# Kernel tuning notes

Measured on AMD Instinct MI355X. Metric: run time of the kernel, lower is better.

Reference implementation:

```python
import jax, jax.numpy as jnp
import numpy as np

# MX microscaling spec: block_size=32 shared power-of-2 scale, int8 elements (MXINT8),
# vector (SIMD) ops rounded to bfloat16 as in microxcaling's simd_* / vec_* ops.
BLOCK = 32
BITS = 8  # int8 element format: grid step 2^(shared_exp - (BITS-2)), range [-2^(BITS-1), 2^(BITS-1)-1]


def bf16_round(x):
    # bfloat=16 rounding used by simd_split / simd_add / vec ops
    return x.astype(jnp.bfloat16).astype(jnp.float32)


def mx_quant(x):
    """MXINT8 fake-quant along last (contraction) axis with block-shared exponent.
    Straight-through estimator for gradients."""
    s = x.shape
    xb = x.reshape(s[:-1] + (s[-1] // BLOCK, BLOCK))
    amax = jnp.max(jnp.abs(xb), axis=-1, keepdims=True)
    shared_exp = jnp.floor(jnp.log2(jnp.where(amax > 0, amax, 1.0)))
    scale = jnp.exp2(shared_exp - (BITS - 2))
    q = jnp.clip(jnp.round(xb / scale), -(2.0 ** (BITS - 1)), 2.0 ** (BITS - 1) - 1) * scale
    q = jnp.where(amax > 0, q, 0.0).reshape(s)
    return x + jax.lax.stop_gradient(q - x)


def mx_linear(x, W, b):
    # quantize activations and weights to MX blocks along K, fp32 accumulate, bf16 bias-add
    y = jnp.einsum('btk,ok->bto', mx_quant(x), mx_quant(W))
    return bf16_round(y + b)


def mx_layernorm(x, w, b, eps=1e-5):
    mu = jnp.mean(x, axis=-1, keepdims=True)
    var = jnp.mean(jnp.square(x - mu), axis=-1, keepdims=True)
    return bf16_round((x - mu) * jax.lax.rsqrt(var + eps) * w + b)


def mx_gelu(x):
    # tanh-approx gelu as in microxcaling, bf16-rounded output
    c = jnp.float32(0.7978845608028654)  # sqrt(2/pi)
    return bf16_round(0.5 * x * (1.0 + jnp.tanh(c * (x + 0.044715 * x * x * x))))


def setup_inputs() -> dict:
    key = jax.random.key(0)
    ks = jax.random.split(key, 5)
    B, S, H = 2, 2048, 2048
    inputs = jax.random.normal(ks[0], (B, S, H), dtype=jnp.float32)
    ln_w = jnp.ones((H,), dtype=jnp.float32)
    ln_b = jnp.zeros((H,), dtype=jnp.float32)
    W1 = jax.random.normal(ks[1], (4 * H, H), dtype=jnp.float32) * (1.0 / np.sqrt(H))
    b1 = jnp.zeros((4 * H,), dtype=jnp.float32)
    W2 = jax.random.normal(ks[2], (H, 4 * H), dtype=jnp.float32) * (1.0 / np.sqrt(4 * H))
    b2 = jnp.zeros((H,), dtype=jnp.float32)
    return {"inputs": inputs, "ln_w": ln_w, "ln_b": ln_b, "W1": W1, "b1": b1, "W2": W2, "b2": b2}


def reference(inputs, ln_w, ln_b, W1, b1, W2, b2):
    # simd_split: bf16-rounded copies for MLP branch and residual branch
    x = bf16_round(inputs)
    residual = bf16_round(inputs)
    h = mx_layernorm(x, ln_w, ln_b)
    h = mx_linear(h, W1, b1)          # [B,S,4H]
    h = mx_gelu(h)
    h = mx_linear(h, W2, b2)          # [B,S,H]
    return bf16_round(residual + h)    # simd_add
```

## Files before the change

kernel.cpp:

```cpp
#include <hip/hip_runtime.h>

#define DEVI __device__ __forceinline__

typedef __bf16 bf16x8 __attribute__((ext_vector_type(8)));
typedef float f32x4 __attribute__((ext_vector_type(4)));

DEVI unsigned short f2bf(float f) {
  unsigned u = __float_as_uint(f);
  u = (u + 0x7FFFu + ((u >> 16) & 1u)) >> 16;
  return (unsigned short)u;
}
DEVI float bf2f(unsigned short h) { return __uint_as_float(((unsigned)h) << 16); }
DEVI float bf16r(float f) { return bf2f(f2bf(f)); }

DEVI void mx_scales(float amax, float& scale, float& inv) {
  unsigned eb = __float_as_uint(amax) & 0x7f800000u;
  scale = __uint_as_float(eb - (6u << 23));
  inv   = __uint_as_float((260u << 23) - eb);
}

DEVI unsigned short quantv(float v, float scale, float inv) {
  float qv = rintf(v * inv);
  qv = fminf(fmaxf(qv, -128.f), 127.f);
  return f2bf(qv * scale);
}

DEVI void quant8(const float* h, float amax, unsigned short* q) {
  if (amax > 0.f) {
    float scale, inv;
    mx_scales(amax, scale, inv);
#pragma unroll
    for (int k = 0; k < 8; ++k) q[k] = quantv(h[k], scale, inv);
  } else {
#pragma unroll
    for (int k = 0; k < 8; ++k) q[k] = 0;
  }
}

template <int N>
DEVI float qmax_step(float x) {
  int y = __builtin_amdgcn_update_dpp(0, __float_as_int(x), 0x120 | N, 0xF, 0xF, true);
  return fmaxf(x, __int_as_float(y));
}
DEVI float quad_row_max(float x) {
  x = qmax_step<1>(x);
  x = qmax_step<2>(x);
  x = qmax_step<4>(x);
  x = qmax_step<8>(x);
  return x;
}

DEVI void gl2lds16(const void* g, void* l) {
  __builtin_amdgcn_global_load_lds(
      (__attribute__((address_space(1))) void*)const_cast<void*>(g),
      (__attribute__((address_space(3))) void*)l, 16, 0, 0);
}

DEVI uint4 pack8(const unsigned short* q) {
  uint4 o;
  o.x = (unsigned)q[0] | ((unsigned)q[1] << 16);
  o.y = (unsigned)q[2] | ((unsigned)q[3] << 16);
  o.z = (unsigned)q[4] | ((unsigned)q[5] << 16);
  o.w = (unsigned)q[6] | ((unsigned)q[7] << 16);
  return o;
}

__global__ __launch_bounds__(256) void prep_k(const float* __restrict__ W1,
                                              const float* __restrict__ W2,
                                              const float* __restrict__ X,
                                              const float* __restrict__ lw,
                                              const float* __restrict__ lb,
                                              unsigned short* __restrict__ qW1,
                                              unsigned short* __restrict__ qW2,
                                              unsigned short* __restrict__ a1) {
  __shared__ float red[4];
  const int bid = blockIdx.x;
  const int t = threadIdx.x;
  if (bid < 16384) {
    const float* src = (bid < 8192) ? W1 : W2;
    unsigned short* dst = (bid < 8192) ? qW1 : qW2;
    size_t idx = (size_t)(bid & 8191) * 256 + t;
    float4 v0 = ((const float4*)src)[idx * 2];
    float4 v1 = ((const float4*)src)[idx * 2 + 1];
    float h[8] = {v0.x, v0.y, v0.z, v0.w, v1.x, v1.y, v1.z, v1.w};
    float amax = 0.f;
#pragma unroll
    for (int k = 0; k < 8; ++k) amax = fmaxf(amax, fabsf(h[k]));
    amax = fmaxf(amax, __shfl_xor(amax, 1));
    amax = fmaxf(amax, __shfl_xor(amax, 2));
    unsigned short q[8];
    quant8(h, amax, q);
    ((uint4*)dst)[idx] = pack8(q);
  } else {
    const int H = 2048;
    const int row = bid - 16384;
    const int lane = t & 63, wave = t >> 6;
    const float* xr = X + (size_t)row * H;
    float4 v0 = ((const float4*)xr)[2 * t];
    float4 v1 = ((const float4*)xr)[2 * t + 1];
    float x[8] = {bf16r(v0.x), bf16r(v0.y), bf16r(v0.z), bf16r(v0.w),
                  bf16r(v1.x), bf16r(v1.y), bf16r(v1.z), bf16r(v1.w)};
    float s = 0.f;
#pragma unroll
    for (int k = 0; k < 8; ++k) s += x[k];
#pragma unroll
    for (int o = 32; o; o >>= 1) s += __shfl_xor(s, o);
    if (lane == 0) red[wave] = s;
    __syncthreads();
    float mu = (red[0] + red[1] + red[2] + red[3]) * (1.0f / H);
    __syncthreads();
    float v = 0.f;
#pragma unroll
    for (int k = 0; k < 8; ++k) { float d = x[k] - mu; v += d * d; }
#pragma unroll
    for (int o = 32; o; o >>= 1) v += __shfl_xor(v, o);
    if (lane == 0) red[wave] = v;
    __syncthreads();
    float var = (red[0] + red[1] + red[2] + red[3]) * (1.0f / H);
    float rstd = 1.0f / sqrtf(var + 1e-5f);
    float h[8];
    float amax = 0.f;
#pragma unroll
    for (int k = 0; k < 8; ++k) {
      int col = t * 8 + k;
      h[k] = bf16r((x[k] - mu) * rstd * lw[col] + lb[col]);
      amax = fmaxf(amax, fabsf(h[k]));
    }
    amax = fmaxf(amax, __shfl_xor(amax, 1));
    amax = fmaxf(amax, __shfl_xor(amax, 2));
    unsigned short q[8];
    quant8(h, amax, q);
    ((uint4*)(a1 + (size_t)row * H))[t] = pack8(q);
  }
}

template <int MODE>
__global__ __launch_bounds__(512, 2) void gemm_mx(const unsigned short* __restrict__ A,
                                                  const unsigned short* __restrict__ B,
                                                  int M, int N, int K,
                                                  const float* __restrict__ bias,
                                                  const float* __restrict__ resid,
                                                  void* __restrict__ outp) {
  __shared__ __align__(16) unsigned short As[3][2][128 * 32];
  __shared__ __align__(16) unsigned short Bs[3][2][256 * 32];

  const int tid = threadIdx.x;
  const int lane = tid & 63;
  const int wave = tid >> 6;
  const int lr = lane & 15;
  const int quad = lane >> 4;
  const int wr = (wave >> 2) * 64;
  const int wc = (wave & 3) * 64;

  const int m0 = blockIdx.y * 128;
  const int n0 = blockIdx.x * 256;

  const int xsw = (quad ^ (lr & 3)) << 3;
  const int lro = (wr + lr) * 32 + xsw;
  const int lco = (wc + lr) * 32 + xsw;

  const int sr = tid >> 2;
  const int sc = ((tid & 3) ^ (sr & 3)) << 3;
  const size_t aoff  = (size_t)(m0 + sr) * K + sc;
  const size_t boff0 = (size_t)(n0 + sr) * K + sc;
  const size_t boff1 = (size_t)(n0 + 128 + sr) * K + sc;
  const int lbase = (tid & ~63) * 8;

  const int NT = K >> 6;

  f32x4 acc[4][4];
#pragma unroll
  for (int i = 0; i < 4; ++i)
#pragma unroll
    for (int j = 0; j < 4; ++j) acc[i][j] = (f32x4){0.f, 0.f, 0.f, 0.f};

#pragma unroll
  for (int pt = 0; pt < 2; ++pt)
#pragma unroll
    for (int s = 0; s < 2; ++s) {
      const size_t kadd = (size_t)pt * 64 + s * 32;
      gl2lds16(A + aoff + kadd, &As[pt][s][lbase]);
      gl2lds16(B + boff0 + kadd, &Bs[pt][s][lbase]);
      gl2lds16(B + boff1 + kadd, &Bs[pt][s][4096 + lbase]);
    }
  asm volatile("s_waitcnt vmcnt(6)" ::: "memory");
  __builtin_amdgcn_s_barrier();

  int buf = 0;
  for (int t = 0; t < NT; ++t) {
    int nbuf = buf + 2; if (nbuf >= 3) nbuf -= 3;
    const bool pf = (t + 2) < NT;
#pragma unroll
    for (int s = 0; s < 2; ++s) {
      bf16x8 af[4], bfr[4];
      const unsigned short* Ap = &As[buf][s][0];
      const unsigned short* Bp = &Bs[buf][s][0];
#pragma unroll
      for (int i = 0; i < 4; ++i) af[i] = *(const bf16x8*)(Ap + lro + i * 512);
#pragma unroll
      for (int j = 0; j < 4; ++j) bfr[j] = *(const bf16x8*)(Bp + lco + j * 512);
      if (pf) {
        const size_t kadd = (size_t)(t + 2) * 64 + s * 32;
        gl2lds16(A + aoff + kadd, &As[nbuf][s][lbase]);
        gl2lds16(B + boff0 + kadd, &Bs[nbuf][s][lbase]);
        gl2lds16(B + boff1 + kadd, &Bs[nbuf][s][4096 + lbase]);
      }
      __builtin_amdgcn_s_barrier();
      asm volatile("s_waitcnt lgkmcnt(0)" ::: "memory");
      __builtin_amdgcn_sched_barrier(0);
      __builtin_amdgcn_s_setprio(1);
#pragma unroll
      for (int i = 0; i < 4; ++i)
#pragma unroll
        for (int j = 0; j < 4; ++j)
          acc[i][j] = __builtin_amdgcn_mfma_f32_16x16x32_bf16(af[i], bfr[j], acc[i][j], 0, 0, 0);
      __builtin_amdgcn_s_setprio(0);
      if (s == 1) {
        if (pf) asm volatile("s_waitcnt vmcnt(6)" ::: "memory");
        else    asm volatile("s_waitcnt vmcnt(0)" ::: "memory");
      }
      __builtin_amdgcn_s_barrier();
    }
    if (++buf == 3) buf = 0;
  }

  if (MODE == 1) {
#pragma unroll
    for (int i = 0; i < 4; ++i) {
#pragma unroll
      for (int r = 0; r < 4; ++r) {
        const int gm = m0 + wr + i * 16 + quad * 4 + r;
        float g[4];
#pragma unroll
        for (int j = 0; j < 4; ++j) {
          float tt = bf16r(acc[i][j][r] + bias[n0 + wc + j * 16 + lr]);
          float u = 0.7978845608028654f * (tt + 0.044715f * tt * tt * tt);
          g[j] = bf16r(0.5f * tt * (1.0f + tanhf(u)));
        }
        float a = quad_row_max(fmaxf(fabsf(g[0]), fabsf(g[1])));
        float b = quad_row_max(fmaxf(fabsf(g[2]), fabsf(g[3])));
        unsigned short q[4];
        if (a > 0.f) {
          float sc2, iv; mx_scales(a, sc2, iv);
          q[0] = quantv(g[0], sc2, iv); q[1] = quantv(g[1], sc2, iv);
        } else { q[0] = q[1] = 0; }
        if (b > 0.f) {
          float sc2, iv; mx_scales(b, sc2, iv);
          q[2] = quantv(g[2], sc2, iv); q[3] = quantv(g[3], sc2, iv);
        } else { q[2] = q[3] = 0; }
        unsigned short* orow = (unsigned short*)outp + (size_t)gm * N + n0 + wc + lr;
#pragma unroll
        for (int j = 0; j < 4; ++j) orow[j * 16] = q[j];
      }
    }
  } else {
#pragma unroll
    for (int i = 0; i < 4; ++i) {
#pragma unroll
      for (int j = 0; j < 4; ++j) {
#pragma unroll
        for (int r = 0; r < 4; ++r) {
          int gm = m0 + wr + i * 16 + quad * 4 + r;
          int gn = n0 + wc + j * 16 + lr;
          float h = bf16r(acc[i][j][r] + bias[gn]);
          float rr = bf16r(resid[(size_t)gm * N + gn]);
          ((float*)outp)[(size_t)gm * N + gn] = bf16r(rr + h);
        }
      }
    }
  }
  (void)M;
}

extern "C" void kernel_launch(void* const* d_in, const int* in_sizes, int n_in,
                              void* d_out, int out_size, void* d_ws, size_t ws_size,
                              hipStream_t stream) {
  const float* inputs = (const float*)d_in[0];
  const float* ln_w   = (const float*)d_in[1];
  const float* ln_b   = (const float*)d_in[2];
  const float* W1     = (const float*)d_in[3];
  const float* b1     = (const float*)d_in[4];
  const float* W2     = (const float*)d_in[5];
  const float* b2     = (const float*)d_in[6];
  float* out = (float*)d_out;
  char* ws = (char*)d_ws;
  (void)in_sizes; (void)n_in; (void)out_size; (void)ws_size;

  unsigned short* qW1  = (unsigned short*)(ws);
  unsigned short* qW2  = (unsigned short*)(ws + (size_t)33554432);
  unsigned short* a1   = (unsigned short*)(ws + (size_t)67108864);
  unsigned short* act2 = (unsigned short*)(ws + (size_t)83886080);

  const int M = 4096;

  prep_k<<<20480, 256, 0, stream>>>(W1, W2, inputs, ln_w, ln_b, qW1, qW2, a1);

  gemm_mx<1><<<dim3(8192 / 256, M / 128), 512, 0, stream>>>(
      a1, qW1, M, 8192, 2048, b1, nullptr, (void*)act2);

  gemm_mx<2><<<dim3(2048 / 256, M / 128), 512, 0, stream>>>(
      act2, qW2, M, 2048, 8192, b2, inputs, (void*)out);
}
```

Baseline: 558.4 us.

## Use 64-wide K tiles in LDS with 8-chunk XOR swizzle for global loads

Changes the shared-memory layout from two 32-wide K halves per stage to a single 64-wide row per stage, with an 8-way XOR swizzle on 16-byte chunks. Each thread now loads 8 consecutive lanes' worth of a 128-byte row segment, which gives longer contiguous global reads per row. The two MFMA sub-steps read the chunk pairs chA and chA^4. The intent is better global-load coalescing and fewer LDS bank conflicts, at the cost of more address registers and a more complex swizzle.

```diff
diff --git a/kernel.cpp b/kernel.cpp
--- a/kernel.cpp
+++ b/kernel.cpp
@@ -141,8 +141,8 @@
                                                   const float* __restrict__ bias,
                                                   const float* __restrict__ resid,
                                                   void* __restrict__ outp) {
-  __shared__ __align__(16) unsigned short As[3][2][128 * 32];
-  __shared__ __align__(16) unsigned short Bs[3][2][256 * 32];
+  __shared__ __align__(16) unsigned short As[3][128 * 64];
+  __shared__ __align__(16) unsigned short Bs[3][256 * 64];
 
   const int tid = threadIdx.x;
   const int lane = tid & 63;
@@ -155,16 +155,18 @@
   const int m0 = blockIdx.y * 128;
   const int n0 = blockIdx.x * 256;
 
-  const int xsw = (quad ^ (lr & 3)) << 3;
-  const int lro = (wr + lr) * 32 + xsw;
-  const int lco = (wc + lr) * 32 + xsw;
-
-  const int sr = tid >> 2;
-  const int sc = ((tid & 3) ^ (sr & 3)) << 3;
-  const size_t aoff  = (size_t)(m0 + sr) * K + sc;
-  const size_t boff0 = (size_t)(n0 + sr) * K + sc;
-  const size_t boff1 = (size_t)(n0 + 128 + sr) * K + sc;
-  const int lbase = (tid & ~63) * 8;
+  const int chA = quad ^ (lr & 7);
+  const int lroA = (wr + lr) * 64;
+  const int lcoA = (wc + lr) * 64;
+
+  const int sr8 = tid >> 3;
+  const int sch = (tid & 7) ^ (sr8 & 7);
+  size_t aoff[2], boff[4];
+#pragma unroll
+  for (int j = 0; j < 2; ++j) aoff[j] = (size_t)(m0 + j * 64 + sr8) * K + sch * 8;
+#pragma unroll
+  for (int j = 0; j < 4; ++j) boff[j] = (size_t)(n0 + j * 64 + sr8) * K + sch * 8;
+  const int lb = (tid & ~63) * 8;
 
   const int NT = K >> 6;
 
@@ -175,14 +177,13 @@
     for (int j = 0; j < 4; ++j) acc[i][j] = (f32x4){0.f, 0.f, 0.f, 0.f};
 
 #pragma unroll
-  for (int pt = 0; pt < 2; ++pt)
-#pragma unroll
-    for (int s = 0; s < 2; ++s) {
-      const size_t kadd = (size_t)pt * 64 + s * 32;
-      gl2lds16(A + aoff + kadd, &As[pt][s][lbase]);
-      gl2lds16(B + boff0 + kadd, &Bs[pt][s][lbase]);
-      gl2lds16(B + boff1 + kadd, &Bs[pt][s][4096 + lbase]);
-    }
+  for (int pt = 0; pt < 2; ++pt) {
+    const size_t kadd = (size_t)pt * 64;
+#pragma unroll
+    for (int j = 0; j < 2; ++j) gl2lds16(A + aoff[j] + kadd, &As[pt][j * 4096 + lb]);
+#pragma unroll
+    for (int j = 0; j < 4; ++j) gl2lds16(B + boff[j] + kadd, &Bs[pt][j * 4096 + lb]);
+  }
   asm volatile("s_waitcnt vmcnt(6)" ::: "memory");
   __builtin_amdgcn_s_barrier();
 
@@ -190,20 +191,20 @@
   for (int t = 0; t < NT; ++t) {
     int nbuf = buf + 2; if (nbuf >= 3) nbuf -= 3;
     const bool pf = (t + 2) < NT;
-#pragma unroll
-    for (int s = 0; s < 2; ++s) {
+    const size_t kadd = (size_t)(t + 2) * 64;
+
+    {
       bf16x8 af[4], bfr[4];
-      const unsigned short* Ap = &As[buf][s][0];
-      const unsigned short* Bp = &Bs[buf][s][0];
-#pragma unroll
-      for (int i = 0; i < 4; ++i) af[i] = *(const bf16x8*)(Ap + lro + i * 512);
-#pragma unroll
-      for (int j = 0; j < 4; ++j) bfr[j] = *(const bf16x8*)(Bp + lco + j * 512);
+      const unsigned short* Ap = &As[buf][lroA + chA * 8];
+      const unsigned short* Bp = &Bs[buf][lcoA + chA * 8];
+#pragma unroll
+      for (int i = 0; i < 4; ++i) af[i] = *(const bf16x8*)(Ap + i * 1024);
+#pragma unroll
+      for (int j = 0; j < 4; ++j) bfr[j] = *(const bf16x8*)(Bp + j * 1024);
       if (pf) {
-        const size_t kadd = (size_t)(t + 2) * 64 + s * 32;
-        gl2lds16(A + aoff + kadd, &As[nbuf][s][lbase]);
-        gl2lds16(B + boff0 + kadd, &Bs[nbuf][s][lbase]);
-        gl2lds16(B + boff1 + kadd, &Bs[nbuf][s][4096 + lbase]);
+        gl2lds16(A + aoff[0] + kadd, &As[nbuf][lb]);
+        gl2lds16(B + boff[0] + kadd, &Bs[nbuf][lb]);
+        gl2lds16(B + boff[1] + kadd, &Bs[nbuf][4096 + lb]);
       }
       __builtin_amdgcn_s_barrier();
       asm volatile("s_waitcnt lgkmcnt(0)" ::: "memory");
@@ -215,10 +216,34 @@
         for (int j = 0; j < 4; ++j)
           acc[i][j] = __builtin_amdgcn_mfma_f32_16x16x32_bf16(af[i], bfr[j], acc[i][j], 0, 0, 0);
       __builtin_amdgcn_s_setprio(0);
-      if (s == 1) {
-        if (pf) asm volatile("s_waitcnt vmcnt(6)" ::: "memory");
-        else    asm volatile("s_waitcnt vmcnt(0)" ::: "memory");
+      __builtin_amdgcn_s_barrier();
+    }
+
+    {
+      bf16x8 af[4], bfr[4];
+      const unsigned short* Ap = &As[buf][lroA + (chA ^ 4) * 8];
+      const unsigned short* Bp = &Bs[buf][lcoA + (chA ^ 4) * 8];
+#pragma unroll
+      for (int i = 0; i < 4; ++i) af[i] = *(const bf16x8*)(Ap + i * 1024);
+#pragma unroll
+      for (int j = 0; j < 4; ++j) bfr[j] = *(const bf16x8*)(Bp + j * 1024);
+      if (pf) {
+        gl2lds16(A + aoff[1] + kadd, &As[nbuf][4096 + lb]);
+        gl2lds16(B + boff[2] + kadd, &Bs[nbuf][8192 + lb]);
+        gl2lds16(B + boff[3] + kadd, &Bs[nbuf][12288 + lb]);
       }
+      __builtin_amdgcn_s_barrier();
+      asm volatile("s_waitcnt lgkmcnt(0)" ::: "memory");
+      __builtin_amdgcn_sched_barrier(0);
+      __builtin_amdgcn_s_setprio(1);
+#pragma unroll
+      for (int i = 0; i < 4; ++i)
+#pragma unroll
+        for (int j = 0; j < 4; ++j)
+          acc[i][j] = __builtin_amdgcn_mfma_f32_16x16x32_bf16(af[i], bfr[j], acc[i][j], 0, 0, 0);
+      __builtin_amdgcn_s_setprio(0);
+      if (pf) asm volatile("s_waitcnt vmcnt(6)" ::: "memory");
+      else    asm volatile("s_waitcnt vmcnt(0)" ::: "memory");
       __builtin_amdgcn_s_barrier();
     }
     if (++buf == 3) buf = 0;
```

After: 513.4 us. 8.1% less time.

## Enlarge GEMM tiles to 256-row blocks with 4-stage K pipeline and grid swizzle

Applied to the files above, without the earlier changes.

The GEMM kernel is restructured to use 256-row M tiles, with each wave computing 128 rows. It is templated on N width: 256 for the first GEMM and 128 for the second. The K loop now steps by 32 with a 4-buffer pipeline that prefetches three tiles ahead and needs one barrier per iteration instead of two, and the LDS swizzle pattern changes. Workgroup indices are remapped across 8 groups to improve L2 locality. The goal is more MFMA work per LDS load and fewer syncs, at the cost of more accumulator registers and LDS, which may lower occupancy below the launch bound of 2.

```diff
diff --git a/kernel.cpp b/kernel.cpp
--- a/kernel.cpp
+++ b/kernel.cpp
@@ -4,6 +4,8 @@
 
 typedef __bf16 bf16x8 __attribute__((ext_vector_type(8)));
 typedef float f32x4 __attribute__((ext_vector_type(4)));
+
+#define WAIT_VM(n) asm volatile("s_waitcnt vmcnt(" #n ")" ::: "memory")
 
 DEVI unsigned short f2bf(float f) {
   unsigned u = __float_as_uint(f);
@@ -134,106 +136,121 @@
   }
 }
 
-template <int MODE>
+template <int MODE, int NREP>
 __global__ __launch_bounds__(512, 2) void gemm_mx(const unsigned short* __restrict__ A,
                                                   const unsigned short* __restrict__ B,
                                                   int M, int N, int K,
                                                   const float* __restrict__ bias,
                                                   const float* __restrict__ resid,
                                                   void* __restrict__ outp) {
-  __shared__ __align__(16) unsigned short As[3][2][128 * 32];
-  __shared__ __align__(16) unsigned short Bs[3][2][256 * 32];
+  constexpr int BN = NREP * 64;
+  constexpr int BT_B = BN * 32;
+  __shared__ __align__(16) unsigned short As[4 * 256 * 32];
+  __shared__ __align__(16) unsigned short Bs[4 * BT_B];
 
   const int tid = threadIdx.x;
   const int lane = tid & 63;
-  const int wave = tid >> 6;
   const int lr = lane & 15;
   const int quad = lane >> 4;
-  const int wr = (wave >> 2) * 64;
-  const int wc = (wave & 3) * 64;
-
-  const int m0 = blockIdx.y * 128;
-  const int n0 = blockIdx.x * 256;
-
-  const int xsw = (quad ^ (lr & 3)) << 3;
-  const int lro = (wr + lr) * 32 + xsw;
-  const int lco = (wc + lr) * 32 + xsw;
-
-  const int sr = tid >> 2;
-  const int sc = ((tid & 3) ^ (sr & 3)) << 3;
-  const size_t aoff  = (size_t)(m0 + sr) * K + sc;
-  const size_t boff0 = (size_t)(n0 + sr) * K + sc;
-  const size_t boff1 = (size_t)(n0 + 128 + sr) * K + sc;
-  const int lbase = (tid & ~63) * 8;
-
-  const int NT = K >> 6;
-
-  f32x4 acc[4][4];
-#pragma unroll
-  for (int i = 0; i < 4; ++i)
-#pragma unroll
-    for (int j = 0; j < 4; ++j) acc[i][j] = (f32x4){0.f, 0.f, 0.f, 0.f};
-
-#pragma unroll
-  for (int pt = 0; pt < 2; ++pt)
-#pragma unroll
-    for (int s = 0; s < 2; ++s) {
-      const size_t kadd = (size_t)pt * 64 + s * 32;
-      gl2lds16(A + aoff + kadd, &As[pt][s][lbase]);
-      gl2lds16(B + boff0 + kadd, &Bs[pt][s][lbase]);
-      gl2lds16(B + boff1 + kadd, &Bs[pt][s][4096 + lbase]);
-    }
-  asm volatile("s_waitcnt vmcnt(6)" ::: "memory");
+  const int wave = tid >> 6;
+  const int wm = wave >> 2;
+  const int wn = wave & 3;
+
+  const int gx = gridDim.x;
+  const int nwg = gx * gridDim.y;
+  int lin = blockIdx.y * gx + blockIdx.x;
+  lin = (lin & 7) * (nwg >> 3) + (lin >> 3);
+  const int m0 = (lin / gx) * 256;
+  const int n0 = (lin % gx) * BN;
+
+  const int ch = quad ^ ((lr >> 1) & 3);
+  const int arow = (wm * 128 + lr) * 32 + ch * 8;
+  const int brow = (wn * (NREP * 16) + lr) * 32 + ch * 8;
+
+  const int srow = tid >> 2;
+  const int sch = (tid & 3) ^ ((tid >> 3) & 3);
+  const size_t aoffL0 = (size_t)(m0 + srow) * K + sch * 8;
+  const size_t aoffL1 = (size_t)(m0 + 128 + srow) * K + sch * 8;
+  const size_t boffL0 = (size_t)(n0 + srow) * K + sch * 8;
+  size_t boffL1 = 0;
+  if constexpr (NREP == 4) boffL1 = (size_t)(n0 + 128 + srow) * K + sch * 8;
+  const int lb = (tid & ~63) * 8;
+
+  const int NT = K >> 5;
+
+  f32x4 acc[8][NREP];
+#pragma unroll
+  for (int i = 0; i < 8; ++i)
+#pragma unroll
+    for (int j = 0; j < NREP; ++j) acc[i][j] = (f32x4){0.f, 0.f, 0.f, 0.f};
+
+#pragma unroll
+  for (int pt = 0; pt < 3; ++pt) {
+    const size_t kb = (size_t)pt * 32;
+    gl2lds16(A + aoffL0 + kb, As + pt * 8192 + lb);
+    gl2lds16(A + aoffL1 + kb, As + pt * 8192 + 4096 + lb);
+    gl2lds16(B + boffL0 + kb, Bs + pt * BT_B + lb);
+    if constexpr (NREP == 4) gl2lds16(B + boffL1 + kb, Bs + pt * BT_B + 4096 + lb);
+  }
+  if constexpr (NREP == 4) WAIT_VM(8); else WAIT_VM(6);
   __builtin_amdgcn_s_barrier();
 
-  int buf = 0;
   for (int t = 0; t < NT; ++t) {
-    int nbuf = buf + 2; if (nbuf >= 3) nbuf -= 3;
-    const bool pf = (t + 2) < NT;
-#pragma unroll
-    for (int s = 0; s < 2; ++s) {
-      bf16x8 af[4], bfr[4];
-      const unsigned short* Ap = &As[buf][s][0];
-      const unsigned short* Bp = &Bs[buf][s][0];
-#pragma unroll
-      for (int i = 0; i < 4; ++i) af[i] = *(const bf16x8*)(Ap + lro + i * 512);
-#pragma unroll
-      for (int j = 0; j < 4; ++j) bfr[j] = *(const bf16x8*)(Bp + lco + j * 512);
-      if (pf) {
-        const size_t kadd = (size_t)(t + 2) * 64 + s * 32;
-        gl2lds16(A + aoff + kadd, &As[nbuf][s][lbase]);
-        gl2lds16(B + boff0 + kadd, &Bs[nbuf][s][lbase]);
-        gl2lds16(B + boff1 + kadd, &Bs[nbuf][s][4096 + lbase]);
-      }
-      __builtin_amdgcn_s_barrier();
-      asm volatile("s_waitcnt lgkmcnt(0)" ::: "memory");
-      __builtin_amdgcn_sched_barrier(0);
-      __builtin_amdgcn_s_setprio(1);
-#pragma unroll
-      for (int i = 0; i < 4; ++i)
-#pragma unroll
-        for (int j = 0; j < 4; ++j)
-          acc[i][j] = __builtin_amdgcn_mfma_f32_16x16x32_bf16(af[i], bfr[j], acc[i][j], 0, 0, 0);
-      __builtin_amdgcn_s_setprio(0);
-      if (s == 1) {
-        if (pf) asm volatile("s_waitcnt vmcnt(6)" ::: "memory");
-        else    asm volatile("s_waitcnt vmcnt(0)" ::: "memory");
-      }
-      __builtin_amdgcn_s_barrier();
-    }
-    if (++buf == 3) buf = 0;
+    const unsigned short* Ab = As + (t & 3) * 8192;
+    const unsigned short* Bb = Bs + (t & 3) * BT_B;
+    bf16x8 a0[4], a1[4], bq[NREP];
+#pragma unroll
+    for (int i = 0; i < 4; ++i) a0[i] = *(const bf16x8*)(Ab + arow + i * 512);
+#pragma unroll
+    for (int j = 0; j < NREP; ++j) bq[j] = *(const bf16x8*)(Bb + brow + j * 512);
+    const bool pf = (t + 3) < NT;
+    const int nb = (t + 3) & 3;
+    const size_t kb = (size_t)(t + 3) * 32;
+    if (pf) {
+      gl2lds16(A + aoffL0 + kb, As + nb * 8192 + lb);
+      gl2lds16(A + aoffL1 + kb, As + nb * 8192 + 4096 + lb);
+    }
+#pragma unroll
+    for (int i = 0; i < 4; ++i) a1[i] = *(const bf16x8*)(Ab + arow + 2048 + i * 512);
+    if (pf) {
+      gl2lds16(B + boffL0 + kb, Bs + nb * BT_B + lb);
+      if constexpr (NREP == 4) gl2lds16(B + boffL1 + kb, Bs + nb * BT_B + 4096 + lb);
+    }
+    __builtin_amdgcn_s_setprio(1);
+#pragma unroll
+    for (int i = 0; i < 4; ++i)
+#pragma unroll
+      for (int j = 0; j < NREP; ++j)
+        acc[i][j] = __builtin_amdgcn_mfma_f32_16x16x32_bf16(a0[i], bq[j], acc[i][j], 0, 0, 0);
+    __builtin_amdgcn_s_setprio(0);
+    __builtin_amdgcn_s_setprio(1);
+#pragma unroll
+    for (int i = 0; i < 4; ++i)
+#pragma unroll
+      for (int j = 0; j < NREP; ++j)
+        acc[i + 4][j] = __builtin_amdgcn_mfma_f32_16x16x32_bf16(a1[i], bq[j], acc[i + 4][j], 0, 0, 0);
+    __builtin_amdgcn_s_setprio(0);
+    if (pf) {
+      if constexpr (NREP == 4) WAIT_VM(8); else WAIT_VM(6);
+    } else if (t + 2 < NT) {
+      if constexpr (NREP == 4) WAIT_VM(4); else WAIT_VM(3);
+    } else {
+      WAIT_VM(0);
+    }
+    __builtin_amdgcn_s_barrier();
+    __builtin_amdgcn_sched_barrier(0);
   }
 
   if (MODE == 1) {
 #pragma unroll
-    for (int i = 0; i < 4; ++i) {
+    for (int i = 0; i < 8; ++i) {
 #pragma unroll
       for (int r = 0; r < 4; ++r) {
-        const int gm = m0 + wr + i * 16 + quad * 4 + r;
+        const int gm = m0 + wm * 128 + i * 16 + quad * 4 + r;
         float g[4];
 #pragma unroll
         for (int j = 0; j < 4; ++j) {
-          float tt = bf16r(acc[i][j][r] + bias[n0 + wc + j * 16 + lr]);
+          float tt = bf16r(acc[i][j][r] + bias[n0 + wn * 64 + j * 16 + lr]);
           float u = 0.7978845608028654f * (tt + 0.044715f * tt * tt * tt);
           g[j] = bf16r(0.5f * tt * (1.0f + tanhf(u)));
         }
@@ -248,20 +265,20 @@
           float sc2, iv; mx_scales(b, sc2, iv);
           q[2] = quantv(g[2], sc2, iv); q[3] = quantv(g[3], sc2, iv);
         } else { q[2] = q[3] = 0; }
-        unsigned short* orow = (unsigned short*)outp + (size_t)gm * N + n0 + wc + lr;
+        unsigned short* orow = (unsigned short*)outp + (size_t)gm * N + n0 + wn * 64 + lr;
 #pragma unroll
         for (int j = 0; j < 4; ++j) orow[j * 16] = q[j];
       }
     }
   } else {
 #pragma unroll
-    for (int i = 0; i < 4; ++i) {
-#pragma unroll
-      for (int j = 0; j < 4; ++j) {
+    for (int i = 0; i < 8; ++i) {
+#pragma unroll
+      for (int j = 0; j < NREP; ++j) {
 #pragma unroll
         for (int r = 0; r < 4; ++r) {
-          int gm = m0 + wr + i * 16 + quad * 4 + r;
-          int gn = n0 + wc + j * 16 + lr;
+          int gm = m0 + wm * 128 + i * 16 + quad * 4 + r;
+          int gn = n0 + wn * (NREP * 16) + j * 16 + lr;
           float h = bf16r(acc[i][j][r] + bias[gn]);
           float rr = bf16r(resid[(size_t)gm * N + gn]);
           ((float*)outp)[(size_t)gm * N + gn] = bf16r(rr + h);
@@ -295,9 +312,9 @@
 
   prep_k<<<20480, 256, 0, stream>>>(W1, W2, inputs, ln_w, ln_b, qW1, qW2, a1);
 
-  gemm_mx<1><<<dim3(8192 / 256, M / 128), 512, 0, stream>>>(
+  gemm_mx<1, 4><<<dim3(8192 / 256, M / 256), 512, 0, stream>>>(
       a1, qW1, M, 8192, 2048, b1, nullptr, (void*)act2);
 
-  gemm_mx<2><<<dim3(2048 / 256, M / 128), 512, 0, stream>>>(
+  gemm_mx<2, 2><<<dim3(2048 / 128, M / 256), 512, 0, stream>>>(
       act2, qW2, M, 2048, 8192, b2, inputs, (void*)out);
 }
```

Result: no change. 565.4 us (+1.2%).
